# Optimization experiments

Measured on AMD Instinct MI355X. Metric: run time of the kernel, lower is better.

Reference implementation:

```python
import jax, jax.numpy as jnp
import numpy as np


def _gru_layer(x, Wih, Whh, bih, bhh):
    # x: [B, T, F]; Wih: [3H, F]; Whh: [3H, H]; gate order (PyTorch): r, z, n
    B = x.shape[0]
    H = Whh.shape[1]
    xp = jnp.einsum('btf,gf->btg', x, Wih) + bih  # [B, T, 3H], input projections precomputed

    def step(h, xt):
        gh = h @ Whh.T + bhh                      # [B, 3H]
        xr, xz, xn = jnp.split(xt, 3, axis=-1)
        hr, hz, hn = jnp.split(gh, 3, axis=-1)
        r = jax.nn.sigmoid(xr + hr)
        z = jax.nn.sigmoid(xz + hz)
        n = jnp.tanh(xn + r * hn)
        h_new = (1.0 - z) * n + z * h
        return h_new, h_new

    h0 = jnp.zeros((B, H), dtype=x.dtype)
    _, ys = jax.lax.scan(step, h0, jnp.swapaxes(xp, 0, 1))  # scan over time
    return jnp.swapaxes(ys, 0, 1)                            # [B, T, H]


def setup_inputs() -> dict:
    key = jax.random.key(0)
    ks = jax.random.split(key, 16)
    B, T, F, H, O = 64, 512, 128, 512, 128
    s_in = 1.0 / np.sqrt(F)
    s_h = 1.0 / np.sqrt(H)
    inp = {
        'x': jax.random.normal(ks[0], (B, T, F), jnp.float32),
        'Wih0': jax.random.normal(ks[1], (3 * H, F), jnp.float32) * s_in,
        'Whh0': jax.random.normal(ks[2], (3 * H, H), jnp.float32) * s_h,
        'bih0': jax.random.normal(ks[3], (3 * H,), jnp.float32) * s_h,
        'bhh0': jax.random.normal(ks[4], (3 * H,), jnp.float32) * s_h,
        'Wih1': jax.random.normal(ks[5], (3 * H, H), jnp.float32) * s_h,
        'Whh1': jax.random.normal(ks[6], (3 * H, H), jnp.float32) * s_h,
        'bih1': jax.random.normal(ks[7], (3 * H,), jnp.float32) * s_h,
        'bhh1': jax.random.normal(ks[8], (3 * H,), jnp.float32) * s_h,
        'Wih2': jax.random.normal(ks[9], (3 * H, H), jnp.float32) * s_h,
        'Whh2': jax.random.normal(ks[10], (3 * H, H), jnp.float32) * s_h,
        'bih2': jax.random.normal(ks[11], (3 * H,), jnp.float32) * s_h,
        'bhh2': jax.random.normal(ks[12], (3 * H,), jnp.float32) * s_h,
        'Wout': jax.random.normal(ks[13], (O, H), jnp.float32) * s_h,
        'bout': jax.random.normal(ks[14], (O,), jnp.float32) * s_h,
    }
    return inp


def reference(x, Wih0, Whh0, bih0, bhh0, Wih1, Whh1, bih1, bhh1,
              Wih2, Whh2, bih2, bhh2, Wout, bout):
    h = _gru_layer(x, Wih0, Whh0, bih0, bhh0)
    h = _gru_layer(h, Wih1, Whh1, bih1, bhh1)
    h = _gru_layer(h, Wih2, Whh2, bih2, bhh2)
    out = jnp.einsum('bth,oh->bto', h, Wout) + bout  # linear head, output_activation=None
    return out
```

## Files before the change

kernel.cpp:

```cpp
#include <hip/hip_runtime.h>
#include <stdint.h>
#include <math.h>

#define NB 64
#define NT 512
#define NF 128
#define NH 512
#define NO 128
#define HSTR 520

typedef short  s16x8  __attribute__((ext_vector_type(8)));
typedef float  f32x4  __attribute__((ext_vector_type(4)));
typedef float  f32x16 __attribute__((ext_vector_type(16)));

#define OFF_XBF   ((size_t)0)
#define OFF_WOUT  ((size_t)(8u<<20))
#define OFF_SEQ0  ((size_t)(12u<<20))
#define OFF_SEQ1  (OFF_SEQ0 + ((size_t)32u<<20))
#define OFF_SEQ2  (OFF_SEQ1 + ((size_t)32u<<20))
#define OFF_FLAGS (OFF_SEQ2 + ((size_t)32u<<20))

#define SMEM_BYTES 133120

__device__ __forceinline__ unsigned short f2bf(float f) {
  unsigned int u = __float_as_uint(f);
  u += 0x7fffu + ((u >> 16) & 1u);
  return (unsigned short)(u >> 16);
}

__device__ __forceinline__ unsigned int ld_flag(unsigned int* p) {
  return __hip_atomic_load(p, __ATOMIC_RELAXED, __HIP_MEMORY_SCOPE_AGENT);
}

__device__ __forceinline__ void poll4(unsigned int* line, int j, unsigned int tgt) {
  unsigned int* p = line + j*4;
  for (;;) {
    unsigned int a = ld_flag(p+0), b = ld_flag(p+1);
    unsigned int c = ld_flag(p+2), d = ld_flag(p+3);
    unsigned int m = min(min(a,b), min(c,d));
    if (m >= tgt) break;
    __builtin_amdgcn_s_sleep(1);
  }
}

__device__ __forceinline__ float sigmoid_f(float x) { return 1.f / (1.f + __expf(-x)); }
__device__ __forceinline__ float tanh_f(float x)    { return 1.f - 2.f / (__expf(2.f*x) + 1.f); }

__global__ __launch_bounds__(384, 1)
void gru_persist(const unsigned short* __restrict__ xbf,
                 unsigned short* __restrict__ seq0,
                 unsigned short* __restrict__ seq1,
                 unsigned short* __restrict__ seq2,
                 unsigned int* __restrict__ flags,
                 const float* __restrict__ Wih0, const float* __restrict__ Whh0,
                 const float* __restrict__ bih0, const float* __restrict__ bhh0,
                 const float* __restrict__ Wih1, const float* __restrict__ Whh1,
                 const float* __restrict__ bih1, const float* __restrict__ bhh1,
                 const float* __restrict__ Wih2, const float* __restrict__ Whh2,
                 const float* __restrict__ bih2, const float* __restrict__ bhh2)
{
  extern __shared__ char smem[];
  unsigned short* WLs = (unsigned short*)smem;
  unsigned short* xA  = (unsigned short*)(smem + 98304);
  float (*xpL)[3][16][33] = (float (*)[3][16][33])(smem + 114944);
  float (*rzL)[16][33]    = (float (*)[16][33])(smem + 127616);
  unsigned short* hout    = (unsigned short*)(smem + 131840);

  const int tid  = threadIdx.x;
  const int wid  = tid >> 6;
  const int lane = tid & 63;
  const int col  = lane & 15;
  const int quad = lane >> 4;

  const int wg = blockIdx.x;
  const int l  = wg >> 6;
  const int rr = wg & 63;
  const int bq = rr >> 4;
  const int cq = rr & 15;
  const int c0 = cq * 32;
  const int b0 = bq * 16;

  unsigned short* seqw = (l==0) ? seq0 : (l==1) ? seq1 : seq2;
  const unsigned short* seqr = (l==1) ? seq0 : (l==2) ? seq1 : (const unsigned short*)0;

  const bool isrec = (wid < 3);
  const int  g     = isrec ? wid : wid - 3;

  const float* Whh = (l==0)?Whh0:(l==1)?Whh1:Whh2;
  const float* Wih = (l==0)?Wih0:(l==1)?Wih1:Wih2;
  const float* bhh = (l==0)?bhh0:(l==1)?bhh1:bhh2;
  const float* bih = (l==0)?bih0:(l==1)?bih1:bih2;

  const float* Wsrc = isrec ? Whh : Wih;
  const int K   = isrec ? NH : ((l==0) ? NF : NH);
  const int KT  = K >> 5;
  const int KTx = (l==0) ? 4 : 16;
  const int xrow = (l==0) ? NF : NH;

  s16x8 wr0[16], wr1[16];
  if (isrec) {
    #pragma unroll
    for (int kt = 0; kt < 16; ++kt) {
      #pragma unroll
      for (int j = 0; j < 2; ++j) {
        const float* s = Wsrc + (size_t)(g*NH + c0 + j*16 + col) * NH + kt*32 + quad*8;
        s16x8 w;
        #pragma unroll
        for (int jj = 0; jj < 8; ++jj) w[jj] = (short)f2bf(s[jj]);
        *(s16x8*)&WLs[((g*16 + kt)*2 + j)*512 + lane*8] = w;
      }
    }
  } else {
    #pragma unroll
    for (int kt = 0; kt < 16; ++kt) {
      if (kt < KT) {
        const float* s0 = Wsrc + (size_t)(g*NH + c0 +      col) * K + kt*32 + quad*8;
        const float* s1 = Wsrc + (size_t)(g*NH + c0 + 16 + col) * K + kt*32 + quad*8;
        s16x8 w0, w1;
        #pragma unroll
        for (int j = 0; j < 8; ++j) { w0[j] = (short)f2bf(s0[j]); w1[j] = (short)f2bf(s1[j]); }
        wr0[kt] = w0; wr1[kt] = w1;
      } else { wr0[kt] = (s16x8)0; wr1[kt] = (s16x8)0; }
    }
  }
  const float* bb = isrec ? bhh : bih;
  const float bias0 = bb[g*NH + c0 +      col];
  const float bias1 = bb[g*NH + c0 + 16 + col];

  unsigned int* line_self = flags + (size_t)(l*4 + bq)*16;
  unsigned int* line_prev = (l > 0) ? (flags + (size_t)((l-1)*4 + bq)*16) : line_self;

  auto stage_tile = [&](unsigned short* dst, const unsigned short* srcbase,
                        int rowlen, int step, int half) {
    const int sr = (half << 3) + (lane >> 3);
    const int sc = lane & 7;
    const unsigned short* src = srcbase + ((size_t)(b0 + sr)*NT + step)*rowlen;
    const int nld = rowlen >> 6;
    s16x8 tmp[8];
    #pragma unroll
    for (int i = 0; i < 8; ++i) if (i < nld) tmp[i] = *(const s16x8*)(src + (i*8 + sc)*8);
    #pragma unroll
    for (int i = 0; i < 8; ++i) if (i < nld) *(s16x8*)&dst[sr*HSTR + (i*8 + sc)*8] = tmp[i];
  };

  if (!isrec) {
    if (l > 0 && lane < 4) poll4(line_prev, lane, 1u);
    asm volatile("" ::: "memory");
    f32x4 a0 = {0.f,0.f,0.f,0.f}, a1 = {0.f,0.f,0.f,0.f};
    const unsigned short* ar = (l==0)
        ? xbf  + (size_t)(b0+col)*NT*NF + quad*8
        : seqr + (size_t)(b0+col)*NT*NH + quad*8;
    #pragma unroll
    for (int kt = 0; kt < 16; ++kt) if (kt < KTx) {
      s16x8 a = *(const s16x8*)(ar + kt*32);
      a0 = __builtin_amdgcn_mfma_f32_16x16x32_bf16(a, wr0[kt], a0, 0, 0, 0);
      a1 = __builtin_amdgcn_mfma_f32_16x16x32_bf16(a, wr1[kt], a1, 0, 0, 0);
    }
    #pragma unroll
    for (int i = 0; i < 4; ++i) {
      int row = quad*4 + i;
      xpL[0][g][row][col]      = a0[i] + bias0;
      xpL[0][g][row][col + 16] = a1[i] + bias1;
    }
  } else if (wid < 2) {
    if (l > 0 && lane < 4) poll4(line_prev, lane, 2u);
    asm volatile("" ::: "memory");
    stage_tile(xA, (l==0) ? xbf : seqr, xrow, 1, wid);
  }
  __syncthreads();

  float hp0[4] = {0.f,0.f,0.f,0.f}, hp1[4] = {0.f,0.f,0.f,0.f};

  for (int t = 0; t < NT; ++t) {
    const int slot  = t & 1;
    const int nslot = slot ^ 1;

    f32x4 a0 = {0.f,0.f,0.f,0.f}, a1 = {0.f,0.f,0.f,0.f};

    if (isrec) {
      if (t > 0) {
        if (lane < 4) poll4(line_self, lane, (unsigned)t);
        asm volatile("" ::: "memory");
        const unsigned short* hsrc =
            seqw + ((size_t)(b0 + col)*NT + (t - 1))*NH + quad*8;
        s16x8 af[16];
        #pragma unroll
        for (int kt = 0; kt < 16; ++kt) af[kt] = *(const s16x8*)(hsrc + kt*32);
        #pragma unroll
        for (int kt = 0; kt < 16; ++kt) {
          s16x8 b0w = *(const s16x8*)&WLs[((g*16 + kt)*2 + 0)*512 + lane*8];
          s16x8 b1w = *(const s16x8*)&WLs[((g*16 + kt)*2 + 1)*512 + lane*8];
          a0 = __builtin_amdgcn_mfma_f32_16x16x32_bf16(af[kt], b0w, a0, 0, 0, 0);
          a1 = __builtin_amdgcn_mfma_f32_16x16x32_bf16(af[kt], b1w, a1, 0, 0, 0);
        }
      }
      if (g < 2) {
        #pragma unroll
        for (int i = 0; i < 4; ++i) {
          int row = quad*4 + i;
          float p0 = a0[i] + xpL[slot][g][row][col]      + bias0;
          float p1 = a1[i] + xpL[slot][g][row][col + 16] + bias1;
          rzL[g][row][col]      = sigmoid_f(p0);
          rzL[g][row][col + 16] = sigmoid_f(p1);
        }
      } else {
        #pragma unroll
        for (int i = 0; i < 4; ++i) { a0[i] += bias0; a1[i] += bias1; }
      }
    } else if (t + 1 < NT) {
      #pragma unroll
      for (int kt = 0; kt < 16; ++kt) if (kt < KTx) {
        s16x8 a = *(const s16x8*)&xA[col*HSTR + kt*32 + quad*8];
        a0 = __builtin_amdgcn_mfma_f32_16x16x32_bf16(a, wr0[kt], a0, 0, 0, 0);
        a1 = __builtin_amdgcn_mfma_f32_16x16x32_bf16(a, wr1[kt], a1, 0, 0, 0);
      }
      #pragma unroll
      for (int i = 0; i < 4; ++i) {
        int row = quad*4 + i;
        xpL[nslot][g][row][col]      = a0[i] + bias0;
        xpL[nslot][g][row][col + 16] = a1[i] + bias1;
      }
    }
    __syncthreads();

    if (wid == 2) {
      #pragma unroll
      for (int i = 0; i < 4; ++i) {
        int row = quad*4 + i;
        float xn0 = xpL[slot][2][row][col];
        float xn1 = xpL[slot][2][row][col + 16];
        float rt0 = rzL[0][row][col],      rt1 = rzL[0][row][col + 16];
        float zt0 = rzL[1][row][col],      zt1 = rzL[1][row][col + 16];
        float nv0 = tanh_f(xn0 + rt0 * a0[i]);
        float nv1 = tanh_f(xn1 + rt1 * a1[i]);
        float h0 = (1.f - zt0)*nv0 + zt0*hp0[i];
        float h1 = (1.f - zt1)*nv1 + zt1*hp1[i];
        hp0[i] = h0; hp1[i] = h1;
        hout[row*32 + col]      = f2bf(h0);
        hout[row*32 + col + 16] = f2bf(h1);
      }
      asm volatile("s_waitcnt lgkmcnt(0)" ::: "memory");
      {
        int srow = lane >> 2, sch = lane & 3;
        s16x8 hv = *(const s16x8*)&hout[srow*32 + sch*8];
        unsigned short* p = seqw + ((size_t)(b0+srow)*NT + t)*NH + c0 + sch*8;
        asm volatile("global_store_dwordx4 %0, %1, off sc0 sc1" :: "v"(p), "v"(hv) : "memory");
        asm volatile("s_waitcnt vmcnt(0)" ::: "memory");
      }
      if (lane == 0)
        __hip_atomic_store(line_self + cq, (unsigned)(t + 1),
                           __ATOMIC_RELAXED, __HIP_MEMORY_SCOPE_AGENT);
    } else if (wid == 3 || wid == 4) {
      if (t + 2 < NT) {
        if (l > 0 && lane < 4) poll4(line_prev, lane, (unsigned)(t + 3));
        asm volatile("" ::: "memory");
        stage_tile(xA, (l==0) ? xbf : seqr, xrow, t + 2, wid - 3);
      }
    }
    __syncthreads();
  }
}

__global__ __launch_bounds__(256)
void head_gemm(const unsigned short* __restrict__ seq2,
               const unsigned short* __restrict__ woutb,
               const float* __restrict__ bout,
               float* __restrict__ out)
{
  int tid = threadIdx.x;
  int wv = tid >> 6, lane = tid & 63;
  int col = lane & 31, khi = lane >> 5;
  int id = blockIdx.x*4 + wv;
  int mt = id >> 2, nt = id & 3;
  int m0 = mt*32, n0 = nt*32;
  const unsigned short* arow = seq2  + (size_t)(m0 + col)*NH + (khi << 3);
  const unsigned short* brow = woutb + (size_t)(n0 + col)*NH + (khi << 3);
  f32x16 acc;
  #pragma unroll
  for (int i = 0; i < 16; ++i) acc[i] = 0.f;
  #pragma unroll 8
  for (int kt = 0; kt < 32; ++kt) {
    s16x8 a = *(const s16x8*)(arow + kt*16);
    s16x8 b = *(const s16x8*)(brow + kt*16);
    acc = __builtin_amdgcn_mfma_f32_32x32x16_bf16(a, b, acc, 0, 0, 0);
  }
  float bo = bout[n0 + col];
  #pragma unroll
  for (int r = 0; r < 16; ++r) {
    int row = (r & 3) + ((r >> 2) << 3) + (khi << 2);
    out[(size_t)(m0 + row)*NO + n0 + col] = acc[r] + bo;
  }
}

__global__ void cast_f32_bf16(const float* __restrict__ src,
                              unsigned short* __restrict__ dst, int n) {
  int i = blockIdx.x*blockDim.x + threadIdx.x;
  int stride = gridDim.x*blockDim.x;
  for (; i < n; i += stride) dst[i] = f2bf(src[i]);
}

extern "C" void kernel_launch(void* const* d_in, const int* in_sizes, int n_in,
                              void* d_out, int out_size, void* d_ws, size_t ws_size,
                              hipStream_t stream) {
  (void)in_sizes; (void)n_in; (void)out_size; (void)ws_size;
  const float* x    = (const float*)d_in[0];
  const float* Wih0 = (const float*)d_in[1];
  const float* Whh0 = (const float*)d_in[2];
  const float* bih0 = (const float*)d_in[3];
  const float* bhh0 = (const float*)d_in[4];
  const float* Wih1 = (const float*)d_in[5];
  const float* Whh1 = (const float*)d_in[6];
  const float* bih1 = (const float*)d_in[7];
  const float* bhh1 = (const float*)d_in[8];
  const float* Wih2 = (const float*)d_in[9];
  const float* Whh2 = (const float*)d_in[10];
  const float* bih2 = (const float*)d_in[11];
  const float* bhh2 = (const float*)d_in[12];
  const float* Wout = (const float*)d_in[13];
  const float* bout = (const float*)d_in[14];

  char* ws = (char*)d_ws;
  unsigned short* xbf  = (unsigned short*)(ws + OFF_XBF);
  unsigned short* wob  = (unsigned short*)(ws + OFF_WOUT);
  unsigned short* seq0 = (unsigned short*)(ws + OFF_SEQ0);
  unsigned short* seq1 = (unsigned short*)(ws + OFF_SEQ1);
  unsigned short* seq2 = (unsigned short*)(ws + OFF_SEQ2);
  unsigned int*   flg  = (unsigned int*)(ws + OFF_FLAGS);

  (void)hipFuncSetAttribute((const void*)gru_persist,
                            hipFuncAttributeMaxDynamicSharedMemorySize, 160*1024);

  hipMemsetAsync(ws + OFF_FLAGS, 0, 4096, stream);
  cast_f32_bf16<<<512, 256, 0, stream>>>(x, xbf, NB*NT*NF);
  cast_f32_bf16<<<64, 256, 0, stream>>>(Wout, wob, NO*NH);
  gru_persist<<<192, 384, SMEM_BYTES, stream>>>(xbf, seq0, seq1, seq2, flg,
      Wih0, Whh0, bih0, bhh0, Wih1, Whh1, bih1, bhh1, Wih2, Whh2, bih2, bhh2);
  head_gemm<<<1024, 256, 0, stream>>>(seq2, wob, bout, (float*)d_out);
}
```

Measured before the change: 2.667 ms.

## Place each GRU row-group on one XCD and poll replicated ring flags

```diff
diff --git a/kernel.cpp b/kernel.cpp
--- a/kernel.cpp
+++ b/kernel.cpp
@@ -19,6 +19,8 @@
 #define OFF_SEQ1  (OFF_SEQ0 + ((size_t)32u<<20))
 #define OFF_SEQ2  (OFF_SEQ1 + ((size_t)32u<<20))
 #define OFF_FLAGS (OFF_SEQ2 + ((size_t)32u<<20))
+#define RING_BASE 2048
+#define NREP 8
 
 #define SMEM_BYTES 133120
 
@@ -41,6 +43,18 @@
     if (m >= tgt) break;
     __builtin_amdgcn_s_sleep(1);
   }
+}
+
+__device__ __forceinline__ bool ringprobe(unsigned int* ringb, int gid, int slot,
+                                          unsigned int epoch, unsigned int t, int lane) {
+  unsigned int* base = ringb + ((size_t)(gid*16 + slot)*NREP)*16 + lane*4;
+  for (int rep = 0; rep < NREP; ++rep) {
+    volatile unsigned int* p = (volatile unsigned int*)(base + rep*16);
+    unsigned int a = p[0], b = p[1], c = p[2], d = p[3];
+    unsigned int m = min(min(a,b), min(c,d));
+    if ((m >> 10) == epoch && (m & 1023u) >= t) return true;
+  }
+  return false;
 }
 
 __device__ __forceinline__ float sigmoid_f(float x) { return 1.f / (1.f + __expf(-x)); }
@@ -72,13 +86,21 @@
   const int col  = lane & 15;
   const int quad = lane >> 4;
 
-  const int wg = blockIdx.x;
-  const int l  = wg >> 6;
-  const int rr = wg & 63;
-  const int bq = rr >> 4;
-  const int cq = rr & 15;
+  const int bid  = blockIdx.x;
+  const int pxcd = bid & 7;
+  if (pxcd >= 6) return;
+  const int wslot = bid >> 3;
+  const int gid  = pxcd*2 + (wslot >> 4);
+  const int cq   = wslot & 15;
+  const int l    = gid >> 2;
+  const int bq   = gid & 3;
   const int c0 = cq * 32;
   const int b0 = bq * 16;
+
+  unsigned int* ringb     = flags + RING_BASE;
+  unsigned int* line_self = flags + (size_t)gid*16;
+  unsigned int* line_prev = (l > 0) ? (flags + (size_t)(gid-4)*16) : line_self;
+  const unsigned int epoch = ld_flag(flags + 1536) & 0x3FFFFFu;
 
   unsigned short* seqw = (l==0) ? seq0 : (l==1) ? seq1 : seq2;
   const unsigned short* seqr = (l==1) ? seq0 : (l==2) ? seq1 : (const unsigned short*)0;
@@ -126,9 +148,6 @@
   const float* bb = isrec ? bhh : bih;
   const float bias0 = bb[g*NH + c0 +      col];
   const float bias1 = bb[g*NH + c0 + 16 + col];
-
-  unsigned int* line_self = flags + (size_t)(l*4 + bq)*16;
-  unsigned int* line_prev = (l > 0) ? (flags + (size_t)((l-1)*4 + bq)*16) : line_self;
 
   auto stage_tile = [&](unsigned short* dst, const unsigned short* srcbase,
                         int rowlen, int step, int half) {
@@ -170,6 +189,8 @@
   __syncthreads();
 
   float hp0[4] = {0.f,0.f,0.f,0.f}, hp1[4] = {0.f,0.f,0.f,0.f};
+  int  ringmiss = 0;
+  bool ringdead = false;
 
   for (int t = 0; t < NT; ++t) {
     const int slot  = t & 1;
@@ -179,7 +200,14 @@
 
     if (isrec) {
       if (t > 0) {
-        if (lane < 4) poll4(line_self, lane, (unsigned)t);
+        if (lane < 4) {
+          bool ok = false;
+          if (!ringdead) ok = ringprobe(ringb, gid, t & 15, epoch, (unsigned)t, lane);
+          if (!ok) {
+            poll4(line_self, lane, (unsigned)t);
+            if (++ringmiss > 8) ringdead = true;
+          } else ringmiss = 0;
+        }
         asm volatile("" ::: "memory");
         const unsigned short* hsrc =
             seqw + ((size_t)(b0 + col)*NT + (t - 1))*NH + quad*8;
@@ -220,6 +248,8 @@
         xpL[nslot][g][row][col]      = a0[i] + bias0;
         xpL[nslot][g][row][col + 16] = a1[i] + bias1;
       }
+      if ((wid == 3 || wid == 4) && l > 0 && t + 2 < NT && lane < 4)
+        poll4(line_prev, lane, (unsigned)(t + 3));
     }
     __syncthreads();
 
@@ -247,18 +277,28 @@
         asm volatile("global_store_dwordx4 %0, %1, off sc0 sc1" :: "v"(p), "v"(hv) : "memory");
         asm volatile("s_waitcnt vmcnt(0)" ::: "memory");
       }
-      if (lane == 0)
+      if (lane == 0) {
+        unsigned int fv = (epoch << 10) | (unsigned)(t + 1);
+        unsigned int* rl = ringb + ((size_t)(gid*16 + ((t+1) & 15))*NREP)*16 + cq;
+        #pragma unroll
+        for (int rep = 0; rep < NREP; ++rep)
+          *(volatile unsigned int*)(rl + rep*16) = fv;
         __hip_atomic_store(line_self + cq, (unsigned)(t + 1),
                            __ATOMIC_RELAXED, __HIP_MEMORY_SCOPE_AGENT);
+      }
     } else if (wid == 3 || wid == 4) {
       if (t + 2 < NT) {
-        if (l > 0 && lane < 4) poll4(line_prev, lane, (unsigned)(t + 3));
         asm volatile("" ::: "memory");
         stage_tile(xA, (l==0) ? xbf : seqr, xrow, t + 2, wid - 3);
       }
     }
     __syncthreads();
   }
+}
+
+__global__ void bump_epoch(unsigned int* p) {
+  if (threadIdx.x == 0 && blockIdx.x == 0)
+    (void)__hip_atomic_fetch_add(p, 1u, __ATOMIC_RELAXED, __HIP_MEMORY_SCOPE_AGENT);
 }
 
 __global__ __launch_bounds__(256)
@@ -331,9 +371,10 @@
                             hipFuncAttributeMaxDynamicSharedMemorySize, 160*1024);
 
   hipMemsetAsync(ws + OFF_FLAGS, 0, 4096, stream);
+  bump_epoch<<<1, 64, 0, stream>>>(flg + 1536);
   cast_f32_bf16<<<512, 256, 0, stream>>>(x, xbf, NB*NT*NF);
   cast_f32_bf16<<<64, 256, 0, stream>>>(Wout, wob, NO*NH);
-  gru_persist<<<192, 384, SMEM_BYTES, stream>>>(xbf, seq0, seq1, seq2, flg,
+  gru_persist<<<256, 384, SMEM_BYTES, stream>>>(xbf, seq0, seq1, seq2, flg,
       Wih0, Whh0, bih0, bhh0, Wih1, Whh1, bih1, bhh1, Wih2, Whh2, bih2, bhh2);
   head_gemm<<<1024, 256, 0, stream>>>(seq2, wob, bout, (float*)d_out);
 }
```

Result: slower. 3.740 ms (+40.2%).
